# Performance work log

Hardware: AMD Instinct MI355X
Metric: run time of the kernel (lower is better)

The kernel has to match this reference:

```python
import jax, jax.numpy as jnp
import numpy as np

MAX_SEQ = 4096
HEADS = 4
LOCAL_HEADS = 1
WINDOW = 128
B, N, D_IN, D, D_OUT = 8, 3000, 128, 512, 64


def setup_inputs():
    key = jax.random.key(0)
    ks = jax.random.split(key, 9)
    s = 0.02
    return {
        'x': jax.random.normal(ks[0], (B, N, D_IN), jnp.float32),
        'W1': jax.random.normal(ks[1], (D_IN, D), jnp.float32) * s,
        'b1': jnp.zeros((D,), jnp.float32),
        'ln1_g': jnp.ones((D,), jnp.float32),
        'ln1_b': jnp.zeros((D,), jnp.float32),
        'Wq': jax.random.normal(ks[2], (D, D), jnp.float32) * s,
        'Wk': jax.random.normal(ks[3], (D, D), jnp.float32) * s,
        'Wv': jax.random.normal(ks[4], (D, D), jnp.float32) * s,
        'Wo': jax.random.normal(ks[5], (D, D), jnp.float32) * s,
        'bo': jnp.zeros((D,), jnp.float32),
        'ln2_g': jnp.ones((D,), jnp.float32),
        'ln2_b': jnp.zeros((D,), jnp.float32),
        'Wf1': jax.random.normal(ks[6], (D, 4 * D), jnp.float32) * s,
        'bf1': jnp.zeros((4 * D,), jnp.float32),
        'Wf2': jax.random.normal(ks[7], (4 * D, D), jnp.float32) * s,
        'bf2': jnp.zeros((D,), jnp.float32),
        'W2': jax.random.normal(ks[8], (D, D_OUT), jnp.float32) * s,
        'b2': jnp.zeros((D_OUT,), jnp.float32),
    }


def _ln(x, g, b, eps=1e-5):
    mu = jnp.mean(x, -1, keepdims=True)
    var = jnp.var(x, -1, keepdims=True)
    return (x - mu) * jax.lax.rsqrt(var + eps) * g + b


def _look_around(x, pad_value=0.0):
    # x: [b, w, n, ...] -> [b, w, 3n, ...] (backward=1, self, forward=1 windows)
    pads = [(0, 0), (1, 1)] + [(0, 0)] * (x.ndim - 2)
    p = jnp.pad(x, pads, constant_values=pad_value)
    w = x.shape[1]
    return jnp.concatenate([p[:, i:i + w] for i in range(3)], axis=2)


def _local_attn(q, k, v):
    # windowed softmax attention, window=128, look back/forward 1 window
    Bh, H, T, d = q.shape
    w = T // WINDOW
    merge = lambda t: t.reshape(Bh * H, w, WINDOW, d)
    bq, bk, bv = merge(q), merge(k), merge(v)
    bk = _look_around(bk)
    bv = _look_around(bv)
    ticker = jnp.arange(T).reshape(1, w, WINDOW)
    bq_k = _look_around(ticker, pad_value=-1)  # [1, w, 3*WINDOW]
    dots = jnp.einsum('bwie,bwje->bwij', bq, bk) * (d ** -0.5)
    mask = (bq_k[:, :, None, :] == -1)
    dots = jnp.where(mask, jnp.finfo(dots.dtype).min, dots)
    attn = jax.nn.softmax(dots, axis=-1)
    out = jnp.einsum('bwij,bwje->bwie', attn, bv)
    return out.reshape(Bh, H, T, d)


def _linear_attn(q, k, v):
    # kernelized global attention: softmax feature maps + d x d context
    d = q.shape[-1]
    q = jax.nn.softmax(q, axis=-1) * (d ** -0.5)
    k = jax.nn.softmax(k, axis=-2)
    ctx = jnp.einsum('bhnd,bhne->bhde', k, v)
    return jnp.einsum('bhnd,bhde->bhne', q, ctx)


def _self_attn(x, Wq, Wk, Wv, Wo, bo):
    Bx, T, Dm = x.shape
    dh = Dm // HEADS
    split = lambda t: t.reshape(Bx, T, HEADS, dh).transpose(0, 2, 1, 3)
    q, k, v = split(x @ Wq), split(x @ Wk), split(x @ Wv)
    lq, gq = q[:, :LOCAL_HEADS], q[:, LOCAL_HEADS:]
    lk, gk = k[:, :LOCAL_HEADS], k[:, LOCAL_HEADS:]
    lv, gv = v[:, :LOCAL_HEADS], v[:, LOCAL_HEADS:]
    local_out = _local_attn(lq, lk, lv)
    global_out = _linear_attn(gq, gk, gv)
    out = jnp.concatenate([local_out, global_out], axis=1)
    out = out.transpose(0, 2, 1, 3).reshape(Bx, T, Dm)
    return out @ Wo + bo


def _forward(x, W1, b1, ln1_g, ln1_b, Wq, Wk, Wv, Wo, bo,
             ln2_g, ln2_b, Wf1, bf1, Wf2, bf2, W2, b2):
    Bx, n, _ = x.shape
    xp = jnp.pad(x, ((0, 0), (0, MAX_SEQ - n), (0, 0)))
    h = jnp.tanh(xp @ W1 + b1)
    # depth=1 transformer block: PreNorm attn + residual, PreNorm FF + residual
    h = h + _self_attn(_ln(h, ln1_g, ln1_b), Wq, Wk, Wv, Wo, bo)
    ff = jax.nn.gelu(_ln(h, ln2_g, ln2_b) @ Wf1 + bf1, approximate=False)
    h = h + ff @ Wf2 + bf2
    out = h @ W2 + b2
    return out[:, :n, :]


def reference(x, W1, b1, ln1_g, ln1_b, Wq, Wk, Wv, Wo, bo,
              ln2_g, ln2_b, Wf1, bf1, Wf2, bf2, W2, b2):
    return _forward(x, W1, b1, ln1_g, ln1_b, Wq, Wk, Wv, Wo, bo,
                    ln2_g, ln2_b, Wf1, bf1, Wf2, bf2, W2, b2)
```

## Files before the change

kernel.cpp:

```cpp
#include <hip/hip_runtime.h>
#include <hip/hip_bf16.h>
#include <math.h>


typedef __hip_bfloat16 bf16;
typedef __attribute__((ext_vector_type(8))) short short8;
typedef __attribute__((ext_vector_type(4))) float floatx4;

#define SEQ   4096
#define NBAT  8
#define DM    512
#define DINP  128
#define DFF   2048
#define NREAL 3000
#define CS    40

#define MFMA16(a,b,c) __builtin_amdgcn_mfma_f32_16x16x32_bf16((a),(b),(c),0,0,0)
#define BARRIER() asm volatile("s_barrier" ::: "memory")

__device__ __forceinline__ void gload_lds16(const void* g, void* l) {
  auto* gp = reinterpret_cast<const __attribute__((address_space(1))) unsigned int*>(
      reinterpret_cast<uintptr_t>(g));
  auto* lp = reinterpret_cast<__attribute__((address_space(3))) unsigned int*>(
      reinterpret_cast<uintptr_t>(l));
  __builtin_amdgcn_global_load_lds(gp, lp, 16, 0, 0);
}

__device__ __forceinline__ short8 lds_read128(const bf16* p) {
  auto* lp = reinterpret_cast<const __attribute__((address_space(3))) bf16*>(
      reinterpret_cast<uintptr_t>(p));
  short8 r;
  asm volatile("ds_read_b128 %0, %1" : "=v"(r) : "v"(lp));
  return r;
}

__device__ __forceinline__ float fast_erff(float x) {
  float ax = fabsf(x);
  float t = __builtin_amdgcn_rcpf(fmaf(0.3275911f, ax, 1.f));
  float p = fmaf(fmaf(fmaf(fmaf(1.061405429f, t, -1.453152027f), t,
                           1.421413741f), t, -0.284496736f), t, 0.254829592f) * t;
  float r = 1.f - p * __expf(-ax * ax);
  return copysignf(r, x);
}

__device__ __forceinline__ float fast_tanhf(float x) {
  float e = __expf(2.f * x);
  return 1.f - 2.f * __builtin_amdgcn_rcpf(e + 1.f);
}

__global__ __launch_bounds__(256) void beacon(float* __restrict__ out, long n) {
  long i = (long)blockIdx.x * 256 + threadIdx.x;
  if (i < n) out[i] = 10000.f;
}

__global__ __launch_bounds__(256) void transpose8(
    const float* __restrict__ W1, const float* __restrict__ Wq,
    const float* __restrict__ Wk, const float* __restrict__ Wv,
    const float* __restrict__ Wo, const float* __restrict__ Wf1,
    const float* __restrict__ Wf2, const float* __restrict__ W2,
    bf16* __restrict__ wt) {
  const int Ks[8]   = {128, 512, 512, 512, 512, 512, 2048, 512};
  const int Ns[8]   = {512, 512, 512, 512, 512, 2048, 512, 64};
  const int Nps[8]  = {512, 512, 512, 512, 512, 2048, 512, 128};
  const long Ofs[8] = {0L, 65536L, 327680L, 589824L, 851968L, 1114112L, 2162688L, 3211264L};
  int zi = blockIdx.z;
  int K = Ks[zi], N = Ns[zi], Npad = Nps[zi];
  int k0 = blockIdx.x * 64, n0 = blockIdx.y * 64;
  if (k0 >= K || n0 >= Npad) return;
  const float* W = zi == 0 ? W1 : zi == 1 ? Wq : zi == 2 ? Wk : zi == 3 ? Wv
                 : zi == 4 ? Wo : zi == 5 ? Wf1 : zi == 6 ? Wf2 : W2;
  bf16* Wt = wt + Ofs[zi];
  __shared__ float t[64][65];
  int r = threadIdx.x >> 2, c = (threadIdx.x & 3) * 16;
#pragma unroll
  for (int i = 0; i < 16; i++) {
    int n = n0 + c + i;
    t[r][c + i] = (n < N) ? W[(long)(k0 + r) * N + n] : 0.f;
  }
  __syncthreads();
#pragma unroll
  for (int i = 0; i < 16; i++)
    Wt[(long)(n0 + r) * K + k0 + c + i] = (bf16)t[c + i][r];
}

__device__ inline uint4 pack8(const float* p) {
  union { bf16 h[8]; uint4 u; } r;
  float4 a = *(const float4*)p;
  float4 b = *(const float4*)(p + 4);
  r.h[0] = (bf16)a.x; r.h[1] = (bf16)a.y; r.h[2] = (bf16)a.z; r.h[3] = (bf16)a.w;
  r.h[4] = (bf16)b.x; r.h[5] = (bf16)b.y; r.h[6] = (bf16)b.z; r.h[7] = (bf16)b.w;
  return r.u;
}

__global__ __launch_bounds__(512, 2) void gemm256(
    const bf16* __restrict__ A, const bf16* __restrict__ Bt,
    const float* __restrict__ bias, float* __restrict__ Cf, bf16* __restrict__ Cb,
    int K, int lda, int ldb, int ldc, int EPI,
    long aBatch, long bBatch, int zdiv, long cOuter, long cInner) {
  __shared__ __align__(16) bf16 sm[2][2][256 * 64];
  const int tid = threadIdx.x;
  const int lane = tid & 63, wid = tid >> 6;

  const int nx = gridDim.x, ny = gridDim.y;
  const long nwg = (long)nx * ny * gridDim.z;
  const long fid = blockIdx.x + (long)nx * (blockIdx.y + (long)ny * blockIdx.z);
  const long cq = nwg >> 3, cr = nwg & 7;
  const long xcd = fid & 7, ofs = fid >> 3;
  const long swz = (xcd < cr ? xcd * (cq + 1) : cr * (cq + 1) + (xcd - cr) * cq) + ofs;
  const int bx = (int)(swz % nx);
  const int by = (int)((swz / nx) % ny);
  const int bz = (int)(swz / ((long)nx * ny));

  const bf16* Ab = A + (long)bz * aBatch;
  const bf16* Bb = Bt + (long)bz * bBatch;
  const long cOff = (long)(bz / zdiv) * cOuter + (long)(bz % zdiv) * cInner;
  const int row0 = by * 256;
  const int col0 = bx * 256;

  const int widm = wid >> 2, widn = wid & 3;
  const int lr = lane & 15, lq4 = lane >> 4;
  const int sw = (lr & 7) << 4;
  const int k0e = ((0 * 64 + lq4 * 16) ^ sw) >> 1;
  const int k1e = ((1 * 64 + lq4 * 16) ^ sw) >> 1;

  const int lrow = lane >> 3;
  const int lch = (lane & 7) ^ lrow;
  const bf16* pAbase = Ab + (long)(row0 + wid * 8 + lrow) * lda + lch * 8;
  const bf16* pBbase = Bb + (long)(col0 + wid * 8 + lrow) * ldb + lch * 8;
  const long a64 = (long)64 * lda, b64 = (long)64 * ldb;
  int kA = 0, kB = 0;

  floatx4 acc[8][4];
#pragma unroll
  for (int i = 0; i < 8; i++)
#pragma unroll
    for (int j = 0; j < 4; j++) acc[i][j] = {0.f, 0.f, 0.f, 0.f};

  auto stageA = [&](int buf, int h) {
    bf16* d = &sm[buf][0][(h * 128 + wid * 8) * 64];
    const bf16* g = pAbase + (long)(h * 2) * a64 + kA;
    gload_lds16(g, d);
    gload_lds16(g + a64, d + 64 * 64);
  };
  auto stageB = [&](int buf, int h) {
    bf16* d = &sm[buf][1][(h * 128 + wid * 8) * 64];
    const bf16* g = pBbase + (long)(h * 2) * b64 + kB;
    gload_lds16(g, d);
    gload_lds16(g + b64, d + 64 * 64);
  };

  short8 bfr[4][2], af[2][2];
  auto readB = [&](int buf) {
    const bf16* base = &sm[buf][1][0];
#pragma unroll
    for (int nt = 0; nt < 4; nt++) {
      int colB = widn * 64 + nt * 16 + lr;
      bfr[nt][0] = lds_read128(base + colB * 64 + k0e);
      bfr[nt][1] = lds_read128(base + colB * 64 + k1e);
    }
  };
  auto readA = [&](int buf, int q) {
    const bf16* base = &sm[buf][0][0];
#pragma unroll
    for (int m = 0; m < 2; m++) {
      int rowA = widm * 128 + q * 32 + m * 16 + lr;
      af[m][0] = lds_read128(base + rowA * 64 + k0e);
      af[m][1] = lds_read128(base + rowA * 64 + k1e);
    }
  };
  auto mmaq = [&](int q) {
    asm volatile("s_waitcnt lgkmcnt(0)" ::: "memory");
    __builtin_amdgcn_sched_barrier(0);
    __builtin_amdgcn_s_setprio(1);
#pragma unroll
    for (int m = 0; m < 2; m++)
#pragma unroll
      for (int nt = 0; nt < 4; nt++) {
        acc[q * 2 + m][nt] = MFMA16(af[m][0], bfr[nt][0], acc[q * 2 + m][nt]);
        acc[q * 2 + m][nt] = MFMA16(af[m][1], bfr[nt][1], acc[q * 2 + m][nt]);
      }
    __builtin_amdgcn_s_setprio(0);
  };

  const int T = K >> 6;
  stageA(0, 0); stageA(0, 1); kA += 64;
  stageB(0, 0); stageB(0, 1); kB += 64;
  stageB(1, 0); stageB(1, 1); kB += 64;
  asm volatile("s_waitcnt vmcnt(4)" ::: "memory");
  BARRIER();

  for (int t = 0; t < T; t++) {
    const int cb = t & 1, nb = cb ^ 1;
    readB(cb);
    readA(cb, 0);
    if (t + 1 < T) stageA(nb, 0);
    mmaq(0);
    BARRIER();
    readA(cb, 1);
    if (t + 1 < T) { stageA(nb, 1); kA += 64; }
    if (t + 2 < T) stageB(cb, 0);
    mmaq(1);
    readA(cb, 2);
    if (t + 2 < T) { stageB(cb, 1); kB += 64; }
    mmaq(2);
    readA(cb, 3);
    mmaq(3);
    if (t + 2 < T) {
      asm volatile("s_waitcnt vmcnt(4)" ::: "memory");
    } else if (t + 1 < T) {
      asm volatile("s_waitcnt vmcnt(0)" ::: "memory");
    }
    BARRIER();
  }

  if (EPI == 2) {
#pragma unroll
    for (int nt = 0; nt < 4; nt++) {
      int c = col0 + widn * 64 + nt * 16 + lr;
      float bv = bias ? bias[c] : 0.f;
#pragma unroll
      for (int mi = 0; mi < 8; mi++) {
        long rb = row0 + widm * 128 + mi * 16 + lq4 * 4;
#pragma unroll
        for (int reg = 0; reg < 4; reg++) {
          float v = acc[mi][nt][reg] + bv;
          long idx = cOff + (rb + reg) * (long)ldc + c;
          Cf[idx] += v;
        }
      }
    }
  } else {
    bf16* scr = ((bf16*)&sm[0][0][0]) + wid * (64 * 72);
    const int rr = lane >> 3, ccol = (lane & 7) * 8;
#pragma unroll
    for (int p = 0; p < 2; p++) {
#pragma unroll
      for (int nt = 0; nt < 4; nt++) {
        int c = col0 + widn * 64 + nt * 16 + lr;
        float bv = bias ? bias[c] : 0.f;
#pragma unroll
        for (int ml = 0; ml < 4; ml++) {
#pragma unroll
          for (int reg = 0; reg < 4; reg++) {
            float v = acc[p * 4 + ml][nt][reg] + bv;
            if (EPI == 4) v = 0.5f * v * (1.f + fast_erff(v * 0.70710678118654752f));
            scr[(ml * 16 + lq4 * 4 + reg) * 72 + nt * 16 + lr] = (bf16)v;
          }
        }
      }
#pragma unroll
      for (int it = 0; it < 8; it++) {
        int r = it * 8 + rr;
        uint4 v = *(const uint4*)&scr[r * 72 + ccol];
        long grow = row0 + widm * 128 + p * 64 + r;
        *(uint4*)&Cb[cOff + grow * (long)ldc + col0 + widn * 64 + ccol] = v;
      }
    }
  }
}

__global__ __launch_bounds__(256) void gemm_bt(
    const void* __restrict__ Avoid, const bf16* __restrict__ Bt,
    const float* __restrict__ bias, float* __restrict__ Cf, bf16* __restrict__ Cb,
    int K, int lda, int ldb, int ldc, int EPI, int AMODE,
    long aBatch, long bBatch, int zdiv, long cOuter, long cInner) {
  __shared__ __align__(16) bf16 As0[128 * 32];
  __shared__ __align__(16) bf16 As1[128 * 32];
  __shared__ __align__(16) bf16 Bs0[128 * 32];
  __shared__ __align__(16) bf16 Bs1[128 * 32];
  const int tid = threadIdx.x;

  const int nx = gridDim.x, ny = gridDim.y;
  const long nwg = (long)nx * ny * gridDim.z;
  const long fid = blockIdx.x + (long)nx * (blockIdx.y + (long)ny * blockIdx.z);
  const long cq = nwg >> 3, cr = nwg & 7;
  const long xcd = fid & 7, ofs = fid >> 3;
  const long swz = (xcd < cr ? xcd * (cq + 1) : cr * (cq + 1) + (xcd - cr) * cq) + ofs;
  const int bx = (int)(swz % nx);
  const int by = (int)((swz / nx) % ny);
  const int bz = (int)(swz / ((long)nx * ny));

  Bt += (long)bz * bBatch;
  const long cOff = (long)(bz / zdiv) * cOuter + (long)(bz % zdiv) * cInner;
  const int row0 = by * 128;
  const int col0 = bx * 128;
  const int lane = tid & 63, wid = tid >> 6;
  const int wm = (wid & 1) * 64, wn = (wid >> 1) * 64;
  const int lr = lane & 15, lk = (lane >> 4) * 8;

  floatx4 acc[4][4];
#pragma unroll
  for (int i = 0; i < 4; i++)
#pragma unroll
    for (int j = 0; j < 4; j++) acc[i][j] = {0.f, 0.f, 0.f, 0.f};

  if (AMODE == 0) {
    const bf16* A = (const bf16*)Avoid + (long)bz * aBatch;
    const bf16* pAa = A + (long)(row0 + wid * 16 + (lane >> 2)) * lda + (lane & 3) * 8;
    const bf16* pBa = Bt + (long)(col0 + wid * 16 + (lane >> 2)) * ldb + (lane & 3) * 8;
    bf16* ldsA0 = &As0[wid * 16 * 32];
    bf16* ldsA1 = &As1[wid * 16 * 32];
    bf16* ldsB0 = &Bs0[wid * 16 * 32];
    bf16* ldsB1 = &Bs1[wid * 16 * 32];
    const long a64 = (long)64 * lda, b64 = (long)64 * ldb;

    auto stage = [&](bf16* dA, bf16* dB) {
      gload_lds16(pAa, dA);
      gload_lds16(pAa + a64, dA + 64 * 32);
      gload_lds16(pBa, dB);
      gload_lds16(pBa + b64, dB + 64 * 32);
      pAa += 32; pBa += 32;
    };
    auto compute = [&](const bf16* AS, const bf16* BS) {
      short8 af[4], bfr[4];
#pragma unroll
      for (int mt = 0; mt < 4; mt++) af[mt] = *(const short8*)(&AS[(wm + mt * 16 + lr) * 32 + lk]);
#pragma unroll
      for (int nt = 0; nt < 4; nt++) bfr[nt] = *(const short8*)(&BS[(wn + nt * 16 + lr) * 32 + lk]);
#pragma unroll
      for (int mt = 0; mt < 4; mt++)
#pragma unroll
        for (int nt = 0; nt < 4; nt++)
          acc[mt][nt] = MFMA16(af[mt], bfr[nt], acc[mt][nt]);
    };

    stage(ldsA0, ldsB0);
    __syncthreads();
    for (int k0 = 0; k0 < K; k0 += 64) {
      stage(ldsA1, ldsB1);
      compute(As0, Bs0);
      __syncthreads();
      if (k0 + 64 < K) stage(ldsA0, ldsB0);
      compute(As1, Bs1);
      __syncthreads();
    }
  } else {
    const float* Af = (const float*)Avoid;
    const int srow = tid >> 2;
    const int skcol = (tid & 3) * 8;
    const long r0 = row0 + srow, r1 = r0 + 64;
    const bf16* pB = Bt + (long)(col0 + srow) * ldb + skcol;
    const int ldsOff = srow * 32 + skcol;
    const float* pF0; const float* pF1;
    bool v0 = true, v1 = true;
    if (AMODE == 1) {
      int t0 = (int)(r0 & (SEQ - 1)), t1 = (int)(r1 & (SEQ - 1));
      v0 = t0 < NREAL; v1 = t1 < NREAL;
      if (!v0) t0 = 0;
      if (!v1) t1 = 0;
      pF0 = Af + ((r0 >> 12) * NREAL + t0) * DINP + skcol;
      pF1 = Af + ((r1 >> 12) * NREAL + t1) * DINP + skcol;
    } else {
      pF0 = Af + r0 * lda + skcol;
      pF1 = Af + r1 * lda + skcol;
    }
    for (int k0 = 0; k0 < K; k0 += 32) {
      uint4 b0 = *(const uint4*)(pB);
      uint4 b1 = *(const uint4*)(pB + (long)64 * ldb);
      pB += 32;
      uint4 a0 = {0, 0, 0, 0}, a1 = {0, 0, 0, 0};
      if (v0) a0 = pack8(pF0);
      if (v1) a1 = pack8(pF1);
      pF0 += 32; pF1 += 32;
      __syncthreads();
      *(uint4*)(&As0[ldsOff]) = a0;
      *(uint4*)(&As0[ldsOff + 64 * 32]) = a1;
      *(uint4*)(&Bs0[ldsOff]) = b0;
      *(uint4*)(&Bs0[ldsOff + 64 * 32]) = b1;
      __syncthreads();
      short8 af[4], bfr[4];
#pragma unroll
      for (int mt = 0; mt < 4; mt++) af[mt] = *(const short8*)(&As0[(wm + mt * 16 + lr) * 32 + lk]);
#pragma unroll
      for (int nt = 0; nt < 4; nt++) bfr[nt] = *(const short8*)(&Bs0[(wn + nt * 16 + lr) * 32 + lk]);
#pragma unroll
      for (int mt = 0; mt < 4; mt++)
#pragma unroll
        for (int nt = 0; nt < 4; nt++)
          acc[mt][nt] = MFMA16(af[mt], bfr[nt], acc[mt][nt]);
    }
  }

#pragma unroll
  for (int nt = 0; nt < 4; nt++) {
    int c = col0 + wn + nt * 16 + lr;
    float bv = 0.f;
    if (bias) {
      if (EPI == 5) { if (c < 64) bv = bias[c]; }
      else bv = bias[c];
    }
#pragma unroll
    for (int mt = 0; mt < 4; mt++) {
      long rb = row0 + wm + mt * 16 + (lane >> 4) * 4;
#pragma unroll
      for (int reg = 0; reg < 4; reg++) {
        float v = acc[mt][nt][reg] + bv;
        long ri = rb + reg;
        long idx = cOff + ri * (long)ldc + c;
        if (EPI == 0) Cf[idx] = fast_tanhf(v);
        else if (EPI == 1) Cb[idx] = (bf16)v;
        else if (EPI == 2) Cf[idx] += v;
        else if (EPI == 4) { float g = 0.5f * v * (1.f + fast_erff(v * 0.70710678118654752f)); Cb[idx] = (bf16)g; }
        else if (EPI == 5) {
          int bb = (int)(ri >> 12); int tt = (int)(ri & (SEQ - 1));
          if (tt < NREAL && c < 64) Cf[((long)bb * NREAL + tt) * 64 + c] = v;
        }
      }
    }
  }
}

__global__ __launch_bounds__(256) void ln_kernel(const float* __restrict__ h,
                                                 const float* __restrict__ g,
                                                 const float* __restrict__ bta,
                                                 bf16* __restrict__ out) {
  int wid = threadIdx.x >> 6, lane = threadIdx.x & 63;
  long row = (long)blockIdx.x * 4 + wid;
  const float* src = h + row * DM + lane * 8;
  float4 a = *(const float4*)(src);
  float4 b = *(const float4*)(src + 4);
  float x[8] = {a.x, a.y, a.z, a.w, b.x, b.y, b.z, b.w};
  float s = 0.f, sq = 0.f;
#pragma unroll
  for (int i = 0; i < 8; i++) { s += x[i]; sq += x[i] * x[i]; }
#pragma unroll
  for (int m = 32; m >= 1; m >>= 1) { s += __shfl_xor(s, m, 64); sq += __shfl_xor(sq, m, 64); }
  float mu = s * (1.f / DM);
  float var = sq * (1.f / DM) - mu * mu;
  float rstd = rsqrtf(var + 1e-5f);
  const float* gp = g + lane * 8;
  const float* bp = bta + lane * 8;
  bf16* dst = out + row * DM + lane * 8;
#pragma unroll
  for (int i = 0; i < 8; i++)
    dst[i] = (bf16)((x[i] - mu) * rstd * gp[i] + bp[i]);
}

__global__ __launch_bounds__(256) void local_attn(const bf16* __restrict__ q,
                                                  const bf16* __restrict__ k,
                                                  const bf16* __restrict__ v,
                                                  bf16* __restrict__ att) {
  int half = blockIdx.x, w = blockIdx.y, b = blockIdx.z;
  int tid = threadIdx.x, wid = tid >> 6, lane = tid & 63;
  int lr = lane & 15, lq4 = lane >> 4;
  __shared__ __align__(16) bf16 Ks[32 * 128];
  __shared__ __align__(16) bf16 Vts[128 * 32];
  __shared__ __align__(16) bf16 Ps[4][16 * 32];

  int t0 = w * 128 + half * 64 + wid * 16;
  long qbase = ((long)b * SEQ + t0 + lr) * DM;
  short8 qf[4];
#pragma unroll
  for (int ks = 0; ks < 4; ks++) qf[ks] = *(const short8*)(q + qbase + ks * 32 + lq4 * 8);

  floatx4 Oacc[8];
#pragma unroll
  for (int i = 0; i < 8; i++) Oacc[i] = {0.f, 0.f, 0.f, 0.f};
  float rs[4] = {0.f, 0.f, 0.f, 0.f};

  int keystart = w * 128 - 128;
  for (int ch = 0; ch < 12; ch++) {
    int kb = keystart + ch * 32;
    if (kb < 0 || kb >= SEQ) continue;
    {
      int j = tid >> 3, d = (tid & 7) * 16;
      const bf16* ksrc = k + ((long)b * SEQ + kb + j) * DM + d;
      *(uint4*)(&Ks[j * 128 + d]) = *(const uint4*)(ksrc);
      *(uint4*)(&Ks[j * 128 + d + 8]) = *(const uint4*)(ksrc + 8);
      const bf16* vsrc = v + ((long)b * SEQ + kb + j) * DM + d;
#pragma unroll
      for (int e = 0; e < 16; e++) Vts[(d + e) * 32 + j] = vsrc[e];
    }
    __syncthreads();
    floatx4 s0 = {0.f, 0.f, 0.f, 0.f}, s1 = {0.f, 0.f, 0.f, 0.f};
#pragma unroll
    for (int ks = 0; ks < 4; ks++) {
      short8 kf0 = *(const short8*)(&Ks[(0 + lr) * 128 + ks * 32 + lq4 * 8]);
      short8 kf1 = *(const short8*)(&Ks[(16 + lr) * 128 + ks * 32 + lq4 * 8]);
      s0 = MFMA16(qf[ks], kf0, s0);
      s1 = MFMA16(qf[ks], kf1, s1);
    }
#pragma unroll
    for (int reg = 0; reg < 4; reg++) {
      float e0 = __expf(s0[reg] * 0.08838834764831845f);
      float e1 = __expf(s1[reg] * 0.08838834764831845f);
      rs[reg] += e0 + e1;
      Ps[wid][(lq4 * 4 + reg) * 32 + lr] = (bf16)e0;
      Ps[wid][(lq4 * 4 + reg) * 32 + 16 + lr] = (bf16)e1;
    }
    __syncthreads();
    short8 pf = *(const short8*)(&Ps[wid][lr * 32 + lq4 * 8]);
#pragma unroll
    for (int nt = 0; nt < 8; nt++) {
      short8 vf = *(const short8*)(&Vts[(nt * 16 + lr) * 32 + lq4 * 8]);
      Oacc[nt] = MFMA16(pf, vf, Oacc[nt]);
    }
    __syncthreads();
  }
#pragma unroll
  for (int m = 1; m < 16; m <<= 1)
#pragma unroll
    for (int reg = 0; reg < 4; reg++) rs[reg] += __shfl_xor(rs[reg], m, 64);
  long obase = ((long)b * SEQ + t0 + lq4 * 4) * DM;
#pragma unroll
  for (int nt = 0; nt < 8; nt++)
#pragma unroll
    for (int reg = 0; reg < 4; reg++)
      att[obase + (long)reg * DM + nt * 16 + lr] = (bf16)(Oacc[nt][reg] / rs[reg]);
}

__global__ __launch_bounds__(256) void qp_softmax(const bf16* __restrict__ q, bf16* __restrict__ qp) {
  int wid = threadIdx.x >> 6, lane = threadIdx.x & 63;
  long task = (long)blockIdx.x * 4 + wid;
  int tt = (int)(task & (SEQ - 1));
  int z6 = (int)(task >> 12);
  int lb = z6 / 3, h2 = z6 % 3;
  const bf16* src = q + ((long)lb * SEQ + tt) * DM + (h2 + 1) * 128 + lane * 2;
  float x0 = (float)src[0], x1 = (float)src[1];
  float m = fmaxf(x0, x1);
#pragma unroll
  for (int s = 32; s >= 1; s >>= 1) m = fmaxf(m, __shfl_xor(m, s, 64));
  float e0 = __expf(x0 - m), e1 = __expf(x1 - m);
  float sm = e0 + e1;
#pragma unroll
  for (int s = 32; s >= 1; s >>= 1) sm += __shfl_xor(sm, s, 64);
  float inv = 0.08838834764831845f / sm;
  bf16* dst = qp + task * 128 + lane * 2;
  dst[0] = (bf16)(e0 * inv);
  dst[1] = (bf16)(e1 * inv);
}

__global__ __launch_bounds__(128) void kstats_part(const bf16* __restrict__ k,
                                                   float* __restrict__ part, int lOff) {
  int chunk = blockIdx.x, z = blockIdx.y;
  int lb = z / 3, h2 = z % 3, ch = (h2 + 1) * 128;
  int d = threadIdx.x;
  const bf16* base = k + ((long)lb * SEQ + chunk * 128) * DM + ch + d;
  float m = -1e30f;
#pragma unroll 4
  for (int t = 0; t < 128; t++) m = fmaxf(m, (float)base[(long)t * DM]);
  float l = 0.f;
#pragma unroll 4
  for (int t = 0; t < 128; t++) l += __expf((float)base[(long)t * DM] - m);
  int idx = (z * 32 + chunk) * 128 + d;
  part[idx] = m;
  part[lOff + idx] = l;
}

__global__ __launch_bounds__(128) void kstats_comb(const float* __restrict__ part,
                                                   float* __restrict__ kml, int lOff) {
  int z = blockIdx.x, d = threadIdx.x;
  float M = -1e30f;
#pragma unroll 4
  for (int c = 0; c < 32; c++) M = fmaxf(M, part[(z * 32 + c) * 128 + d]);
  float L = 0.f;
#pragma unroll 4
  for (int c = 0; c < 32; c++) {
    int i = (z * 32 + c) * 128 + d;
    L += part[lOff + i] * __expf(part[i] - M);
  }
  kml[z * 256 + d] = M;
  kml[z * 256 + 128 + d] = L;
}

__global__ __launch_bounds__(256) void ctx_mfma(const bf16* __restrict__ k,
                                                const bf16* __restrict__ v,
                                                const float* __restrict__ kml,
                                                float* __restrict__ part) {
  int chunk = blockIdx.x, z = blockIdx.y;
  int lb = z / 3, h2 = z % 3, ch = (h2 + 1) * 128;
  int tid = threadIdx.x, lane = tid & 63, wid = tid >> 6;
  const int wm = (wid & 1) * 64, wn = (wid >> 1) * 64;
  const int lr = lane & 15, lk = (lane >> 4) * 8;
  __shared__ float ml2[128];
  __shared__ __align__(16) bf16 Vt[128 * CS];
  __shared__ __align__(16) bf16 Kt[128 * CS];
  if (tid < 128)
    ml2[tid] = kml[z * 256 + tid] + logf(kml[z * 256 + 128 + tid]);

  int j = tid >> 3, d0 = (tid & 7) * 16;
  const bf16* vsrc = v + ((long)lb * SEQ + chunk * 512 + j) * DM + ch + d0;
  const bf16* ksrc = k + ((long)lb * SEQ + chunk * 512 + j) * DM + ch + d0;

  floatx4 acc[4][4];
#pragma unroll
  for (int i = 0; i < 4; i++)
#pragma unroll
    for (int jj = 0; jj < 4; jj++) acc[i][jj] = {0.f, 0.f, 0.f, 0.f};

  for (int s = 0; s < 16; s++) {
    union { bf16 h[16]; uint4 u[2]; } va, ka;
    va.u[0] = *(const uint4*)(vsrc); va.u[1] = *(const uint4*)(vsrc + 8);
    ka.u[0] = *(const uint4*)(ksrc); ka.u[1] = *(const uint4*)(ksrc + 8);
    vsrc += (long)32 * DM; ksrc += (long)32 * DM;
    __syncthreads();
#pragma unroll
    for (int e = 0; e < 16; e++) {
      Vt[(d0 + e) * CS + j] = va.h[e];
      Kt[(d0 + e) * CS + j] = (bf16)__expf((float)ka.h[e] - ml2[d0 + e]);
    }
    __syncthreads();
    short8 af[4], bfr[4];
#pragma unroll
    for (int mt = 0; mt < 4; mt++) af[mt] = *(const short8*)(&Vt[(wm + mt * 16 + lr) * CS + lk]);
#pragma unroll
    for (int nt = 0; nt < 4; nt++) bfr[nt] = *(const short8*)(&Kt[(wn + nt * 16 + lr) * CS + lk]);
#pragma unroll
    for (int mt = 0; mt < 4; mt++)
#pragma unroll
      for (int nt = 0; nt < 4; nt++)
        acc[mt][nt] = MFMA16(af[mt], bfr[nt], acc[mt][nt]);
  }

  float* dst = part + ((long)z * 8 + chunk) * 16384;
#pragma unroll
  for (int nt = 0; nt < 4; nt++) {
    int c = wn + nt * 16 + lr;
#pragma unroll
    for (int mt = 0; mt < 4; mt++) {
      int rb = wm + mt * 16 + (lane >> 4) * 4;
#pragma unroll
      for (int reg = 0; reg < 4; reg++)
        dst[(rb + reg) * 128 + c] = acc[mt][nt][reg];
    }
  }
}

__global__ __launch_bounds__(256) void ctx_reduce(const float* __restrict__ part, bf16* __restrict__ ctxT) {
  long i = (long)blockIdx.x * 256 + threadIdx.x;
  int z = (int)(i >> 14);
  int off = (int)(i & 16383);
  float s = 0.f;
#pragma unroll
  for (int c = 0; c < 8; c++) s += part[(((long)z * 8 + c) << 14) + off];
  ctxT[i] = (bf16)s;
}

extern "C" void kernel_launch(void* const* d_in, const int* in_sizes, int n_in,
                              void* d_out, int out_size, void* d_ws, size_t ws_size,
                              hipStream_t stream) {
  float* outp = (float*)d_out;

  long offH = 0;
  int GB = 0;
  long offLNG, offQ, offK, offV, offATT, offCTXP, offCTXT, offKML, offWT, need;
  for (int gb = 8; gb >= 2; gb >>= 1) {
    long sLN = (long)gb * 4194304;
    offLNG = 67108864L;
    offQ   = offLNG + sLN;
    offK   = offQ + sLN;
    offV   = offK + sLN;
    offATT = offV + sLN;
    offCTXP= offATT + sLN;
    offCTXT= offCTXP + (long)gb * 1572864;
    offKML = offCTXT + (long)gb * 98304;
    offWT  = offKML + (long)gb * 3072;
    need   = offWT + 6553600L;
    if ((size_t)need <= ws_size) { GB = gb; break; }
  }
  if (GB == 0) {
    beacon<<<(out_size + 255) / 256, 256, 0, stream>>>(outp, out_size);
    return;
  }
  const int NG = NBAT / GB;
  const long GR = (long)GB * SEQ;
  const int NZ = GB * 3;

  const float* x   = (const float*)d_in[0];
  const float* W1  = (const float*)d_in[1];
  const float* b1  = (const float*)d_in[2];
  const float* g1  = (const float*)d_in[3];
  const float* be1 = (const float*)d_in[4];
  const float* Wq  = (const float*)d_in[5];
  const float* Wk  = (const float*)d_in[6];
  const float* Wv  = (const float*)d_in[7];
  const float* Wo  = (const float*)d_in[8];
  const float* bo  = (const float*)d_in[9];
  const float* g2  = (const float*)d_in[10];
  const float* be2 = (const float*)d_in[11];
  const float* Wf1 = (const float*)d_in[12];
  const float* bf1 = (const float*)d_in[13];
  const float* Wf2 = (const float*)d_in[14];
  const float* bf2 = (const float*)d_in[15];
  const float* W2  = (const float*)d_in[16];
  const float* b2  = (const float*)d_in[17];

  char* ws = (char*)d_ws;
  float* h   = (float*)(ws + offH);
  bf16* lnG  = (bf16*)(ws + offLNG);
  bf16* qp   = (bf16*)(ws + offLNG);
  bf16* qb   = (bf16*)(ws + offQ);
  bf16* kb   = (bf16*)(ws + offK);
  bf16* vb   = (bf16*)(ws + offV);
  bf16* attb = (bf16*)(ws + offATT);
  bf16* ff1g = (bf16*)(ws + offQ);
  float* ctxp= (float*)(ws + offCTXP);
  bf16* ctxT = (bf16*)(ws + offCTXT);
  float* kml = (float*)(ws + offKML);
  bf16* wt   = (bf16*)(ws + offWT);
  bf16* wqt  = wt + 65536;
  bf16* wot  = wt + 851968;
  bf16* wf1t = wt + 1114112;
  bf16* wf2t = wt + 2162688;
  bf16* w2t  = wt + 3211264;
  const int lOff = NZ * 32 * 128;

  transpose8<<<dim3(32, 32, 8), 256, 0, stream>>>(W1, Wq, Wk, Wv, Wo, Wf1, Wf2, W2, wt);

  gemm_bt<<<dim3(4, 256, 1), 256, 0, stream>>>(x, wt, b1, h, nullptr,
      DINP, DINP, DINP, DM, 0, 1, 0, 0, 1, 0, 0);

  for (int g = 0; g < NG; g++) {
    float* hg = h + (long)g * GR * DM;
    ln_kernel<<<(int)(GR / 4), 256, 0, stream>>>(hg, g1, be1, lnG);
    gemm256<<<dim3(2, (int)(GR / 256), 3), 512, 0, stream>>>(lnG, wqt, nullptr, nullptr, qb,
        DM, DM, DM, DM, 1,
        0L, 262144L, 3, 0L, GR * DM);

    local_attn<<<dim3(2, 32, GB), 256, 0, stream>>>(qb, kb, vb, attb);

    qp_softmax<<<NZ * 1024, 256, 0, stream>>>(qb, qp);
    kstats_part<<<dim3(32, NZ), 128, 0, stream>>>(kb, ctxp, lOff);
    kstats_comb<<<NZ, 128, 0, stream>>>(ctxp, kml, lOff);
    ctx_mfma<<<dim3(8, NZ), 256, 0, stream>>>(kb, vb, kml, ctxp);
    ctx_reduce<<<NZ * 64, 256, 0, stream>>>(ctxp, ctxT);
    gemm_bt<<<dim3(1, 32, NZ), 256, 0, stream>>>(qp, ctxT, nullptr, nullptr, attb + 128,
        128, 128, 128, DM, 1, 0,
        (long)SEQ * 128, 16384L, 3, (long)SEQ * DM, 128L);

    gemm256<<<dim3(2, (int)(GR / 256), 1), 512, 0, stream>>>(attb, wot, bo, hg, nullptr,
        DM, DM, DM, DM, 2, 0, 0, 1, 0, 0);
  }

  for (int g = 0; g < NG; g++) {
    float* hg = h + (long)g * GR * DM;
    ln_kernel<<<(int)(GR / 4), 256, 0, stream>>>(hg, g2, be2, lnG);
    gemm256<<<dim3(8, (int)(GR / 256), 1), 512, 0, stream>>>(lnG, wf1t, bf1, nullptr, ff1g,
        DM, DM, DM, DFF, 4, 0, 0, 1, 0, 0);
    gemm256<<<dim3(2, (int)(GR / 256), 1), 512, 0, stream>>>(ff1g, wf2t, bf2, hg, nullptr,
        DFF, DFF, DFF, DM, 2, 0, 0, 1, 0, 0);
  }

  gemm_bt<<<dim3(1, 256, 1), 256, 0, stream>>>(h, w2t, b2, outp, nullptr,
      DM, DM, DM, 64, 5, 2, 0, 0, 1, 0, 0);
}
```

Before: 651.1 us.

## Triple-buffer B tiles in gemm256 to drop the mid-iteration barrier

```diff
diff --git a/kernel.cpp b/kernel.cpp
--- a/kernel.cpp
+++ b/kernel.cpp
@@ -97,7 +97,8 @@
     const float* __restrict__ bias, float* __restrict__ Cf, bf16* __restrict__ Cb,
     int K, int lda, int ldb, int ldc, int EPI,
     long aBatch, long bBatch, int zdiv, long cOuter, long cInner) {
-  __shared__ __align__(16) bf16 sm[2][2][256 * 64];
+  __shared__ __align__(16) bf16 sm[5 * 256 * 64];
+  bf16* const smB = sm + 2 * 16384;
   const int tid = threadIdx.x;
   const int lane = tid & 63, wid = tid >> 6;
 
@@ -136,22 +137,32 @@
 #pragma unroll
     for (int j = 0; j < 4; j++) acc[i][j] = {0.f, 0.f, 0.f, 0.f};
 
-  auto stageA = [&](int buf, int h) {
-    bf16* d = &sm[buf][0][(h * 128 + wid * 8) * 64];
-    const bf16* g = pAbase + (long)(h * 2) * a64 + kA;
-    gload_lds16(g, d);
-    gload_lds16(g + a64, d + 64 * 64);
+  auto stageA4 = [&](int buf) {
+    bf16* base = sm + buf * 16384;
+#pragma unroll
+    for (int h = 0; h < 2; h++) {
+      bf16* d = base + (h * 128 + wid * 8) * 64;
+      const bf16* g = pAbase + (long)(h * 2) * a64 + kA;
+      gload_lds16(g, d);
+      gload_lds16(g + a64, d + 64 * 64);
+    }
+    kA += 64;
   };
-  auto stageB = [&](int buf, int h) {
-    bf16* d = &sm[buf][1][(h * 128 + wid * 8) * 64];
-    const bf16* g = pBbase + (long)(h * 2) * b64 + kB;
-    gload_lds16(g, d);
-    gload_lds16(g + b64, d + 64 * 64);
+  auto stageB4 = [&](int slot) {
+    bf16* base = smB + slot * 16384;
+#pragma unroll
+    for (int h = 0; h < 2; h++) {
+      bf16* d = base + (h * 128 + wid * 8) * 64;
+      const bf16* g = pBbase + (long)(h * 2) * b64 + kB;
+      gload_lds16(g, d);
+      gload_lds16(g + b64, d + 64 * 64);
+    }
+    kB += 64;
   };
 
   short8 bfr[4][2], af[2][2];
-  auto readB = [&](int buf) {
-    const bf16* base = &sm[buf][1][0];
+  auto readB = [&](int slot) {
+    const bf16* base = smB + slot * 16384;
 #pragma unroll
     for (int nt = 0; nt < 4; nt++) {
       int colB = widn * 64 + nt * 16 + lr;
@@ -160,7 +171,7 @@
     }
   };
   auto readA = [&](int buf, int q) {
-    const bf16* base = &sm[buf][0][0];
+    const bf16* base = sm + buf * 16384;
 #pragma unroll
     for (int m = 0; m < 2; m++) {
       int rowA = widm * 128 + q * 32 + m * 16 + lr;
@@ -183,25 +194,23 @@
   };
 
   const int T = K >> 6;
-  stageA(0, 0); stageA(0, 1); kA += 64;
-  stageB(0, 0); stageB(0, 1); kB += 64;
-  stageB(1, 0); stageB(1, 1); kB += 64;
+  stageA4(0);
+  stageB4(0);
+  stageB4(1);
   asm volatile("s_waitcnt vmcnt(4)" ::: "memory");
   BARRIER();
 
+  int bsel = 0;
   for (int t = 0; t < T; t++) {
     const int cb = t & 1, nb = cb ^ 1;
-    readB(cb);
+    readB(bsel);
     readA(cb, 0);
-    if (t + 1 < T) stageA(nb, 0);
+    if (t + 1 < T) stageA4(nb);
     mmaq(0);
-    BARRIER();
     readA(cb, 1);
-    if (t + 1 < T) { stageA(nb, 1); kA += 64; }
-    if (t + 2 < T) stageB(cb, 0);
     mmaq(1);
     readA(cb, 2);
-    if (t + 2 < T) { stageB(cb, 1); kB += 64; }
+    if (t + 2 < T) stageB4(bsel == 0 ? 2 : bsel - 1);
     mmaq(2);
     readA(cb, 3);
     mmaq(3);
@@ -211,6 +220,7 @@
       asm volatile("s_waitcnt vmcnt(0)" ::: "memory");
     }
     BARRIER();
+    bsel = bsel == 2 ? 0 : bsel + 1;
   }
 
   if (EPI == 2) {
@@ -230,7 +240,7 @@
       }
     }
   } else {
-    bf16* scr = ((bf16*)&sm[0][0][0]) + wid * (64 * 72);
+    bf16* scr = sm + wid * (64 * 72);
     const int rr = lane >> 3, ccol = (lane & 7) * 8;
 #pragma unroll
     for (int p = 0; p < 2; p++) {
```

New measurement: 650.2 us. Within noise of the previous version (-0.1%).
